# Performance work log

Hardware: AMD Instinct MI355X
Metric: run time of the kernel (lower is better)

Reference implementation:

```python
import jax, jax.numpy as jnp
import numpy as np

D_MODEL = 1024
N_HEADS = 16
D_HEAD = D_MODEL // N_HEADS


def setup_inputs() -> dict:
    key = jax.random.key(0)
    ks = jax.random.split(key, 9)
    s = 1.0 / np.sqrt(D_MODEL)
    def lin(kw, kb):
        W = jax.random.uniform(kw, (D_MODEL, D_MODEL), jnp.float32, -s, s)
        b = jax.random.uniform(kb, (D_MODEL,), jnp.float32, -s, s)
        return W, b
    Wq, bq = lin(ks[0], ks[1])
    Wk, bk = lin(ks[2], ks[3])
    Wv, bv = lin(ks[4], ks[5])
    Wo, bo = lin(ks[6], ks[7])
    x = jax.random.normal(ks[8], (4, 2048, D_MODEL), jnp.float32)
    return {"x": x, "Wq": Wq, "bq": bq, "Wk": Wk, "bk": bk,
            "Wv": Wv, "bv": bv, "Wo": Wo, "bo": bo}


def reference(x, Wq, bq, Wk, bk, Wv, bv, Wo, bo):
    B, T, C = x.shape
    # torch Linear: y = x @ W.T + b
    Q = x @ Wq.T + bq
    K = x @ Wk.T + bk
    V = x @ Wv.T + bv
    # [B, H, T, Dh]
    Q = Q.reshape(B, T, N_HEADS, D_HEAD).transpose(0, 2, 1, 3)
    K = K.reshape(B, T, N_HEADS, D_HEAD).transpose(0, 2, 1, 3)
    V = V.reshape(B, T, N_HEADS, D_HEAD).transpose(0, 2, 1, 3)
    scale = jnp.float32(np.sqrt(D_HEAD))
    scores = jnp.einsum('bhqd,bhkd->bhqk', Q, K) / scale
    causal = jnp.tril(jnp.ones((T, T), dtype=bool))  # True where allowed
    scores = jnp.where(causal, scores, jnp.float32(-jnp.inf))
    attn = jax.nn.softmax(scores, axis=-1)
    out = jnp.einsum('bhqk,bhkd->bhqd', attn, V)
    out = out.transpose(0, 2, 1, 3).reshape(B, T, C)
    return out @ Wo.T + bo
```

## Files before the change

kernel.cpp:

```cpp
#include <hip/hip_runtime.h>
#include <hip/hip_bf16.h>


typedef float f32x4 __attribute__((ext_vector_type(4)));
typedef __bf16 bf16x8 __attribute__((ext_vector_type(8)));

#define DEVI __device__ __forceinline__

#define QSCALE 0.1803368801111204f

DEVI ushort f2b(float x) {
  __hip_bfloat16 h = __float2bfloat16(x);
  return __builtin_bit_cast(ushort, h);
}

DEVI bf16x8 ldsFrag(const ushort* p) {
  return __builtin_bit_cast(bf16x8, *(const uint4*)p);
}

DEVI f32x4 mfma16(bf16x8 a, bf16x8 b, f32x4 c) {
  return __builtin_amdgcn_mfma_f32_16x16x32_bf16(a, b, c, 0, 0, 0);
}

DEVI void gload_lds16(const ushort* g, ushort* l) {
  __builtin_amdgcn_global_load_lds(
      (const __attribute__((address_space(1))) unsigned int*)g,
      (__attribute__((address_space(3))) unsigned int*)l, 16, 0, 0);
}

__global__ void k_cvt(const float4* __restrict__ in, ushort4* __restrict__ out, int n4) {
  int i = blockIdx.x * 256 + threadIdx.x;
  if (i >= n4) return;
  float4 f = in[i];
  ushort4 o;
  o.x = f2b(f.x); o.y = f2b(f.y); o.z = f2b(f.z); o.w = f2b(f.w);
  out[i] = o;
}

__global__ void k_cvtW(const float4* __restrict__ w0, const float4* __restrict__ w1,
                       const float4* __restrict__ w2, const float4* __restrict__ w3,
                       ushort4* __restrict__ out) {
  const int y = blockIdx.y;
  const float4* src = (y == 0) ? w0 : (y == 1) ? w1 : (y == 2) ? w2 : w3;
  const int i = blockIdx.x * 256 + threadIdx.x;
  float4 f = src[i];
  ushort4 o;
  o.x = f2b(f.x); o.y = f2b(f.y); o.z = f2b(f.z); o.w = f2b(f.w);
  out[y * 262144 + i] = o;
}

template<int MODE>
__global__ __launch_bounds__(256)
void k_gemm(const ushort* __restrict__ A, const ushort* __restrict__ W,
            const float* __restrict__ b0, const float* __restrict__ b1,
            const float* __restrict__ b2, float* __restrict__ outF,
            ushort* __restrict__ oQ, ushort* __restrict__ oK, ushort* __restrict__ oV) {
  __shared__ ushort As[128 * 32];
  __shared__ ushort Bs[128 * 32];
  const int tid = threadIdx.x;
  const int wave = tid >> 6, lane = tid & 63;
  const int col = lane & 15, quad = lane >> 4;
  const int m0 = blockIdx.y * 128, n0 = blockIdx.x * 128;
  const int wm = (wave >> 1) * 64, wn = (wave & 1) * 64;
  f32x4 acc[4][4] = {};

  const int srow = wave * 16 + (lane >> 2);
  const int scol = (lane & 3) * 8;
  const ushort* Ag = A + (m0 + srow) * 1024 + scol;
  const ushort* Wg = W + (n0 + srow) * 1024 + scol;
  ushort* AsBase0 = &As[(wave * 16) * 32];
  ushort* AsBase1 = &As[(64 + wave * 16) * 32];
  ushort* BsBase0 = &Bs[(wave * 16) * 32];
  ushort* BsBase1 = &Bs[(64 + wave * 16) * 32];

  for (int k0 = 0; k0 < 1024; k0 += 32) {
    __syncthreads();
    gload_lds16(Ag + k0,             AsBase0);
    gload_lds16(Ag + 64 * 1024 + k0, AsBase1);
    gload_lds16(Wg + k0,             BsBase0);
    gload_lds16(Wg + 64 * 1024 + k0, BsBase1);
    __syncthreads();

    bf16x8 af[4], bfr[4];
#pragma unroll
    for (int i = 0; i < 4; ++i)
      af[i] = ldsFrag(&As[(wm + i * 16 + col) * 32 + quad * 8]);
#pragma unroll
    for (int j = 0; j < 4; ++j)
      bfr[j] = ldsFrag(&Bs[(wn + j * 16 + col) * 32 + quad * 8]);
#pragma unroll
    for (int i = 0; i < 4; ++i)
#pragma unroll
      for (int j = 0; j < 4; ++j)
        acc[i][j] = mfma16(af[i], bfr[j], acc[i][j]);
  }

  const int matId = (MODE == 0) ? (n0 >> 10) : 0;
  const float* bias = (MODE == 1) ? b0 : (matId == 0 ? b0 : (matId == 1 ? b1 : b2));
  const float sc = (MODE == 0 && matId == 0) ? QSCALE : 1.0f;
  ushort* outB = (MODE == 0) ? (matId == 0 ? oQ : (matId == 1 ? oK : oV)) : nullptr;

#pragma unroll
  for (int j = 0; j < 4; ++j) {
    const int n = n0 + wn + j * 16 + col;
    const int nl = n & 1023;
    const float bn = bias[nl];
#pragma unroll
    for (int i = 0; i < 4; ++i) {
      const int mBase = m0 + wm + i * 16 + quad * 4;
      if (MODE == 1) {
#pragma unroll
        for (int r = 0; r < 4; ++r)
          outF[(mBase + r) * 1024 + n] = acc[i][j][r] + bn;
      } else if (matId < 2) {
        const int h = nl >> 6, dh = nl & 63;
#pragma unroll
        for (int r = 0; r < 4; ++r) {
          const int m = mBase + r;
          const int b = m >> 11, t = m & 2047;
          outB[(((b * 16 + h) * 2048) + t) * 64 + dh] = f2b((acc[i][j][r] + bn) * sc);
        }
      } else {
        const int b = mBase >> 11, t = mBase & 2047;
        const int h = nl >> 6, dh = nl & 63;
        ushort4 pk;
        pk.x = f2b(acc[i][j][0] + bn);
        pk.y = f2b(acc[i][j][1] + bn);
        pk.z = f2b(acc[i][j][2] + bn);
        pk.w = f2b(acc[i][j][3] + bn);
        *(ushort4*)&outB[(((b * 16 + h) * 64) + dh) * 2048 + t] = pk;
      }
    }
  }
}

__global__ __launch_bounds__(256)
void k_attn(const ushort* __restrict__ Q, const ushort* __restrict__ K,
            const ushort* __restrict__ Vt, ushort* __restrict__ AO) {
  __shared__ ushort Ks[2 * 64 * 32];
  __shared__ ushort Vs[2 * 64 * 32];
  __shared__ ushort Ps[4 * 16 * 72];
  const int tid = threadIdx.x;
  const int wave = tid >> 6, lane = tid & 63;
  const int col = lane & 15, quad = lane >> 4;
  const int bh = blockIdx.y;
  const int px = blockIdx.x;
  const ushort* Qg = Q + (size_t)bh * 2048 * 64;
  const ushort* Kg = K + (size_t)bh * 2048 * 64;
  const ushort* Vg = Vt + (size_t)bh * 64 * 2048;

  const int srow = wave * 16 + (lane >> 2);
  const int scol = (lane & 3) * 8;
  ushort* Ks0 = &Ks[(wave * 16) * 32];
  ushort* Ks1 = &Ks[(64 + wave * 16) * 32];
  ushort* Vs0 = &Vs[(wave * 16) * 32];
  ushort* Vs1 = &Vs[(64 + wave * 16) * 32];
  ushort* Pw = &Ps[wave * 16 * 72 + col * 72];

  for (int pp = 0; pp < 2; ++pp) {
    const int t = pp ? (31 - px) : px;
    const int q0 = t * 64;
    const int qw = q0 + wave * 16;

    bf16x8 qf0, qf1;
    {
      const ushort* p = Qg + (qw + col) * 64 + quad * 8;
      qf0 = __builtin_bit_cast(bf16x8, *(const uint4*)p);
      qf1 = __builtin_bit_cast(bf16x8, *(const uint4*)(p + 32));
    }

    float mrow = -1e30f, lsum = 0.0f;
    f32x4 o[4] = {};

    const ushort* kPtr = Kg + srow * 64 + scol;
    const ushort* vPtr = Vg + srow * 2048 + scol;

    for (int it = 0; it <= t; ++it) {
      __syncthreads();
      gload_lds16(kPtr,      Ks0);
      gload_lds16(kPtr + 32, Ks1);
      gload_lds16(vPtr,      Vs0);
      gload_lds16(vPtr + 32, Vs1);
      kPtr += 64 * 64;
      vPtr += 64;
      __syncthreads();

      const bool diag = (it == t);
      const int imax = diag ? wave : 3;

      f32x4 p[4];
      float tmax = -1e30f;
#pragma unroll
      for (int i = 0; i < 4; ++i) {
        if (i > imax) { p[i] = f32x4{0.f, 0.f, 0.f, 0.f}; continue; }
        bf16x8 kf0 = ldsFrag(&Ks[(i * 16 + col) * 32 + quad * 8]);
        bf16x8 kf1 = ldsFrag(&Ks[(64 + i * 16 + col) * 32 + quad * 8]);
        f32x4 z = {0.f, 0.f, 0.f, 0.f};
        f32x4 s = mfma16(kf0, qf0, z);
        s = mfma16(kf1, qf1, s);
        if (diag && i == wave) {
#pragma unroll
          for (int r = 0; r < 4; ++r)
            if (quad * 4 + r > col) s[r] = -1e30f;
        }
#pragma unroll
        for (int r = 0; r < 4; ++r) tmax = fmaxf(tmax, s[r]);
        p[i] = s;
      }
      tmax = fmaxf(tmax, __shfl_xor(tmax, 16));
      tmax = fmaxf(tmax, __shfl_xor(tmax, 32));
      const float mnew = fmaxf(mrow, tmax);
      const float alpha = __builtin_amdgcn_exp2f(mrow - mnew);
      float psum = 0.0f;
#pragma unroll
      for (int i = 0; i < 4; ++i) {
        if (i > imax) continue;
#pragma unroll
        for (int r = 0; r < 4; ++r) {
          const float e = __builtin_amdgcn_exp2f(p[i][r] - mnew);
          p[i][r] = e;
          psum += e;
        }
      }
      psum += __shfl_xor(psum, 16);
      psum += __shfl_xor(psum, 32);
      lsum = alpha * lsum + psum;
      mrow = mnew;
#pragma unroll
      for (int i = 0; i < 4; ++i) o[i] *= alpha;

#pragma unroll
      for (int i = 0; i < 4; ++i) {
        ushort4 pk;
        pk.x = f2b(p[i][0]); pk.y = f2b(p[i][1]);
        pk.z = f2b(p[i][2]); pk.w = f2b(p[i][3]);
        *(ushort4*)&Pw[i * 16 + quad * 4] = pk;
      }

#pragma unroll
      for (int c = 0; c < 2; ++c) {
        bf16x8 pb = ldsFrag(&Pw[c * 32 + quad * 8]);
#pragma unroll
        for (int i = 0; i < 4; ++i) {
          bf16x8 vf = ldsFrag(&Vs[(c * 64 + i * 16 + col) * 32 + quad * 8]);
          o[i] = mfma16(vf, pb, o[i]);
        }
      }
    }

    const float inv = 1.0f / lsum;
    const int b = bh >> 4, h = bh & 15;
    const int tq = q0 + wave * 16 + col;
    ushort* dst = AO + ((size_t)(b * 2048 + tq)) * 1024 + h * 64;
#pragma unroll
    for (int i = 0; i < 4; ++i) {
      ushort4 pk;
      pk.x = f2b(o[i][0] * inv);
      pk.y = f2b(o[i][1] * inv);
      pk.z = f2b(o[i][2] * inv);
      pk.w = f2b(o[i][3] * inv);
      *(ushort4*)&dst[i * 16 + quad * 4] = pk;
    }
  }
}

extern "C" void kernel_launch(void* const* d_in, const int* in_sizes, int n_in,
                              void* d_out, int out_size, void* d_ws, size_t ws_size,
                              hipStream_t stream) {
  const float* x  = (const float*)d_in[0];
  const float* Wq = (const float*)d_in[1];
  const float* bq = (const float*)d_in[2];
  const float* Wk = (const float*)d_in[3];
  const float* bk = (const float*)d_in[4];
  const float* Wv = (const float*)d_in[5];
  const float* bv = (const float*)d_in[6];
  const float* Wo = (const float*)d_in[7];
  const float* bo = (const float*)d_in[8];
  float* out = (float*)d_out;

  char* ws = (char*)d_ws;
  ushort* xb    = (ushort*)ws;
  ushort* Wcat  = (ushort*)(ws + (size_t)16 * 1024 * 1024);
  ushort* Wob   = Wcat + (size_t)3 * 1024 * 1024;
  ushort* Qh    = (ushort*)(ws + (size_t)24 * 1024 * 1024);
  ushort* Kh    = Qh + (size_t)8192 * 1024;
  ushort* Vt    = Kh + (size_t)8192 * 1024;
  ushort* AO    = Vt + (size_t)8192 * 1024;

  k_cvt<<<8192, 256, 0, stream>>>((const float4*)x, (ushort4*)xb, 8192 * 1024 / 4);
  k_cvtW<<<dim3(1024, 4), 256, 0, stream>>>((const float4*)Wq, (const float4*)Wk,
                                            (const float4*)Wv, (const float4*)Wo,
                                            (ushort4*)Wcat);

  k_gemm<0><<<dim3(24, 64), 256, 0, stream>>>(xb, Wcat, bq, bk, bv, nullptr, Qh, Kh, Vt);

  k_attn<<<dim3(16, 64), 256, 0, stream>>>(Qh, Kh, Vt, AO);

  k_gemm<1><<<dim3(8, 64), 256, 0, stream>>>(AO, Wob, bo, nullptr, nullptr, out,
                                             nullptr, nullptr, nullptr);
}
```

Before: 285.5 us.

## Restructure attention to 128-query tiles, MFMA row sums, and swizzled block mapping

Each attention block now handles 128 queries, with two 16-row query sub-tiles per wave, so every staged K/V tile is reused across twice as many queries. Row sums are computed by an MFMA against a ones block appended to the V tile instead of shuffle reductions. Blocks are remapped with a 1D swizzle across XCDs for both GEMMs and attention, and attention gets a launch_bounds occupancy hint. The cost is more registers and LDS per block and lost load balance, since the old pairing of short and long causal tiles is dropped.

```diff
diff --git a/kernel.cpp b/kernel.cpp
--- a/kernel.cpp
+++ b/kernel.cpp
@@ -12,6 +12,12 @@
 DEVI ushort f2b(float x) {
   __hip_bfloat16 h = __float2bfloat16(x);
   return __builtin_bit_cast(ushort, h);
+}
+
+DEVI ushort4 pack4(f32x4 v) {
+  ushort4 o;
+  o.x = f2b(v[0]); o.y = f2b(v[1]); o.z = f2b(v[2]); o.w = f2b(v[3]);
+  return o;
 }
 
 DEVI bf16x8 ldsFrag(const ushort* p) {
@@ -60,7 +66,10 @@
   const int tid = threadIdx.x;
   const int wave = tid >> 6, lane = tid & 63;
   const int col = lane & 15, quad = lane >> 4;
-  const int m0 = blockIdx.y * 128, n0 = blockIdx.x * 128;
+  const int id = blockIdx.x;
+  const int s_ = id >> 3;
+  const int m0 = ((id & 7) * 8 + (s_ & 7)) * 128;
+  const int n0 = (s_ >> 3) * 128;
   const int wm = (wave >> 1) * 64, wn = (wave & 1) * 64;
   f32x4 acc[4][4] = {};
 
@@ -134,132 +143,160 @@
   }
 }
 
-__global__ __launch_bounds__(256)
+__global__ __launch_bounds__(256, 3)
 void k_attn(const ushort* __restrict__ Q, const ushort* __restrict__ K,
             const ushort* __restrict__ Vt, ushort* __restrict__ AO) {
   __shared__ ushort Ks[2 * 64 * 32];
-  __shared__ ushort Vs[2 * 64 * 32];
-  __shared__ ushort Ps[4 * 16 * 72];
+  __shared__ ushort Vs[2 * 80 * 32];
+  __shared__ ushort Ps[4 * 2 * 16 * 72];
   const int tid = threadIdx.x;
   const int wave = tid >> 6, lane = tid & 63;
   const int col = lane & 15, quad = lane >> 4;
-  const int bh = blockIdx.y;
-  const int px = blockIdx.x;
+  const int id = blockIdx.x;
+  const int sl = id >> 3;
+  const int bh = (id & 7) * 8 + (sl & 7);
+  const int t = sl >> 3;
+  const int q0 = t * 128;
   const ushort* Qg = Q + (size_t)bh * 2048 * 64;
   const ushort* Kg = K + (size_t)bh * 2048 * 64;
   const ushort* Vg = Vt + (size_t)bh * 64 * 2048;
 
+  {
+    const int c = tid >> 7, w = tid & 127;
+    const ushort one = 0x3F80;
+    ushort4 zv;
+    if (w < 8) { zv.x = one; zv.y = one; zv.z = one; zv.w = one; }
+    else       { zv.x = 0;   zv.y = 0;   zv.z = 0;   zv.w = 0;   }
+    *(ushort4*)&Vs[c * 2560 + 2048 + w * 4] = zv;
+  }
+
+  bf16x8 qf[2][2];
+#pragma unroll
+  for (int s = 0; s < 2; ++s) {
+    const ushort* p = Qg + (q0 + wave * 32 + s * 16 + col) * 64 + quad * 8;
+    qf[s][0] = __builtin_bit_cast(bf16x8, *(const uint4*)p);
+    qf[s][1] = __builtin_bit_cast(bf16x8, *(const uint4*)(p + 32));
+  }
+
+  float mrow[2] = {-1e30f, -1e30f};
+  f32x4 o[2][4] = {};
+  f32x4 la[2] = {};
+
   const int srow = wave * 16 + (lane >> 2);
   const int scol = (lane & 3) * 8;
+  const ushort* kPtr = Kg + srow * 64 + scol;
+  const ushort* vPtr = Vg + srow * 2048 + scol;
   ushort* Ks0 = &Ks[(wave * 16) * 32];
   ushort* Ks1 = &Ks[(64 + wave * 16) * 32];
   ushort* Vs0 = &Vs[(wave * 16) * 32];
-  ushort* Vs1 = &Vs[(64 + wave * 16) * 32];
-  ushort* Pw = &Ps[wave * 16 * 72 + col * 72];
-
-  for (int pp = 0; pp < 2; ++pp) {
-    const int t = pp ? (31 - px) : px;
-    const int q0 = t * 64;
-    const int qw = q0 + wave * 16;
-
-    bf16x8 qf0, qf1;
-    {
-      const ushort* p = Qg + (qw + col) * 64 + quad * 8;
-      qf0 = __builtin_bit_cast(bf16x8, *(const uint4*)p);
-      qf1 = __builtin_bit_cast(bf16x8, *(const uint4*)(p + 32));
-    }
-
-    float mrow = -1e30f, lsum = 0.0f;
-    f32x4 o[4] = {};
-
-    const ushort* kPtr = Kg + srow * 64 + scol;
-    const ushort* vPtr = Vg + srow * 2048 + scol;
-
-    for (int it = 0; it <= t; ++it) {
-      __syncthreads();
-      gload_lds16(kPtr,      Ks0);
-      gload_lds16(kPtr + 32, Ks1);
-      gload_lds16(vPtr,      Vs0);
-      gload_lds16(vPtr + 32, Vs1);
-      kPtr += 64 * 64;
-      vPtr += 64;
-      __syncthreads();
-
-      const bool diag = (it == t);
-      const int imax = diag ? wave : 3;
-
+  ushort* Vs1 = &Vs[2560 + (wave * 16) * 32];
+  ushort* Pw0 = &Ps[((wave * 2 + 0) * 16 + col) * 72];
+  ushort* Pw1 = &Ps[((wave * 2 + 1) * 16 + col) * 72];
+
+  auto stage = [&]() {
+    gload_lds16(kPtr,      Ks0);
+    gload_lds16(kPtr + 32, Ks1);
+    gload_lds16(vPtr,      Vs0);
+    gload_lds16(vPtr + 32, Vs1);
+    kPtr += 64 * 64;
+    vPtr += 64;
+  };
+
+  auto step = [&](bool masked, int d) {
+    bf16x8 kf[4][2];
+#pragma unroll
+    for (int i = 0; i < 4; ++i) {
+      kf[i][0] = ldsFrag(&Ks[(i * 16 + col) * 32 + quad * 8]);
+      kf[i][1] = ldsFrag(&Ks[(64 + i * 16 + col) * 32 + quad * 8]);
+    }
+#pragma unroll
+    for (int s = 0; s < 2; ++s) {
+      const int exact = masked ? (2 * wave + s - 4 * d) : 99;
       f32x4 p[4];
       float tmax = -1e30f;
 #pragma unroll
       for (int i = 0; i < 4; ++i) {
-        if (i > imax) { p[i] = f32x4{0.f, 0.f, 0.f, 0.f}; continue; }
-        bf16x8 kf0 = ldsFrag(&Ks[(i * 16 + col) * 32 + quad * 8]);
-        bf16x8 kf1 = ldsFrag(&Ks[(64 + i * 16 + col) * 32 + quad * 8]);
-        f32x4 z = {0.f, 0.f, 0.f, 0.f};
-        f32x4 s = mfma16(kf0, qf0, z);
-        s = mfma16(kf1, qf1, s);
-        if (diag && i == wave) {
-#pragma unroll
-          for (int r = 0; r < 4; ++r)
-            if (quad * 4 + r > col) s[r] = -1e30f;
+        if (i <= exact) {
+          f32x4 z = {0.f, 0.f, 0.f, 0.f};
+          f32x4 sv = mfma16(kf[i][0], qf[s][0], z);
+          sv = mfma16(kf[i][1], qf[s][1], sv);
+          if (masked && i == exact) {
+#pragma unroll
+            for (int r = 0; r < 4; ++r)
+              if (quad * 4 + r > col) sv[r] = -1e30f;
+          }
+#pragma unroll
+          for (int r = 0; r < 4; ++r) tmax = fmaxf(tmax, sv[r]);
+          p[i] = sv;
+        } else {
+          p[i] = f32x4{0.f, 0.f, 0.f, 0.f};
         }
-#pragma unroll
-        for (int r = 0; r < 4; ++r) tmax = fmaxf(tmax, s[r]);
-        p[i] = s;
       }
       tmax = fmaxf(tmax, __shfl_xor(tmax, 16));
       tmax = fmaxf(tmax, __shfl_xor(tmax, 32));
-      const float mnew = fmaxf(mrow, tmax);
-      const float alpha = __builtin_amdgcn_exp2f(mrow - mnew);
-      float psum = 0.0f;
+      const float mnew = fmaxf(mrow[s], tmax);
+      const float alpha = __builtin_amdgcn_exp2f(mrow[s] - mnew);
+      mrow[s] = mnew;
 #pragma unroll
       for (int i = 0; i < 4; ++i) {
-        if (i > imax) continue;
-#pragma unroll
-        for (int r = 0; r < 4; ++r) {
-          const float e = __builtin_amdgcn_exp2f(p[i][r] - mnew);
-          p[i][r] = e;
-          psum += e;
+        if (i <= exact) {
+#pragma unroll
+          for (int r = 0; r < 4; ++r)
+            p[i][r] = __builtin_amdgcn_exp2f(p[i][r] - mnew);
         }
       }
-      psum += __shfl_xor(psum, 16);
-      psum += __shfl_xor(psum, 32);
-      lsum = alpha * lsum + psum;
-      mrow = mnew;
-#pragma unroll
-      for (int i = 0; i < 4; ++i) o[i] *= alpha;
-
+      la[s] *= alpha;
+#pragma unroll
+      for (int i = 0; i < 4; ++i) o[s][i] *= alpha;
+      ushort* Pw = s ? Pw1 : Pw0;
+#pragma unroll
+      for (int i = 0; i < 4; ++i)
+        *(ushort4*)&Pw[i * 16 + quad * 4] = pack4(p[i]);
+    }
+#pragma unroll
+    for (int c = 0; c < 2; ++c) {
+      bf16x8 pb0 = ldsFrag(&Pw0[c * 32 + quad * 8]);
+      bf16x8 pb1 = ldsFrag(&Pw1[c * 32 + quad * 8]);
+      bf16x8 vone = ldsFrag(&Vs[(c * 80 + 64 + col) * 32 + quad * 8]);
+      la[0] = mfma16(vone, pb0, la[0]);
+      la[1] = mfma16(vone, pb1, la[1]);
 #pragma unroll
       for (int i = 0; i < 4; ++i) {
-        ushort4 pk;
-        pk.x = f2b(p[i][0]); pk.y = f2b(p[i][1]);
-        pk.z = f2b(p[i][2]); pk.w = f2b(p[i][3]);
-        *(ushort4*)&Pw[i * 16 + quad * 4] = pk;
+        bf16x8 vf = ldsFrag(&Vs[(c * 80 + i * 16 + col) * 32 + quad * 8]);
+        o[0][i] = mfma16(vf, pb0, o[0][i]);
+        o[1][i] = mfma16(vf, pb1, o[1][i]);
       }
-
-#pragma unroll
-      for (int c = 0; c < 2; ++c) {
-        bf16x8 pb = ldsFrag(&Pw[c * 32 + quad * 8]);
-#pragma unroll
-        for (int i = 0; i < 4; ++i) {
-          bf16x8 vf = ldsFrag(&Vs[(c * 64 + i * 16 + col) * 32 + quad * 8]);
-          o[i] = mfma16(vf, pb, o[i]);
-        }
-      }
-    }
-
-    const float inv = 1.0f / lsum;
-    const int b = bh >> 4, h = bh & 15;
-    const int tq = q0 + wave * 16 + col;
-    ushort* dst = AO + ((size_t)(b * 2048 + tq)) * 1024 + h * 64;
+    }
+  };
+
+  const int nfull = 2 * t;
+  for (int it = 0; it < nfull; ++it) {
+    __syncthreads();
+    stage();
+    __syncthreads();
+    step(false, 0);
+  }
+  __syncthreads();
+  stage();
+  __syncthreads();
+  step(true, 0);
+  __syncthreads();
+  stage();
+  __syncthreads();
+  if (wave >= 2) step(true, 1);
+
+  const int b = bh >> 4, h = bh & 15;
+#pragma unroll
+  for (int s = 0; s < 2; ++s) {
+    const float l = __shfl(la[s][0], col);
+    const float inv = 1.0f / l;
+    const int tq = q0 + wave * 32 + s * 16 + col;
+    ushort* dst = AO + (size_t)(b * 2048 + tq) * 1024 + h * 64;
 #pragma unroll
     for (int i = 0; i < 4; ++i) {
-      ushort4 pk;
-      pk.x = f2b(o[i][0] * inv);
-      pk.y = f2b(o[i][1] * inv);
-      pk.z = f2b(o[i][2] * inv);
-      pk.w = f2b(o[i][3] * inv);
-      *(ushort4*)&dst[i * 16 + quad * 4] = pk;
+      f32x4 v = o[s][i];
+      v[0] *= inv; v[1] *= inv; v[2] *= inv; v[3] *= inv;
+      *(ushort4*)&dst[i * 16 + quad * 4] = pack4(v);
     }
   }
 }
@@ -292,10 +329,10 @@
                                             (const float4*)Wv, (const float4*)Wo,
                                             (ushort4*)Wcat);
 
-  k_gemm<0><<<dim3(24, 64), 256, 0, stream>>>(xb, Wcat, bq, bk, bv, nullptr, Qh, Kh, Vt);
-
-  k_attn<<<dim3(16, 64), 256, 0, stream>>>(Qh, Kh, Vt, AO);
-
-  k_gemm<1><<<dim3(8, 64), 256, 0, stream>>>(AO, Wob, bo, nullptr, nullptr, out,
-                                             nullptr, nullptr, nullptr);
-}
+  k_gemm<0><<<1536, 256, 0, stream>>>(xb, Wcat, bq, bk, bv, nullptr, Qh, Kh, Vt);
+
+  k_attn<<<1024, 256, 0, stream>>>(Qh, Kh, Vt, AO);
+
+  k_gemm<1><<<512, 256, 0, stream>>>(AO, Wob, bo, nullptr, nullptr, out,
+                                     nullptr, nullptr, nullptr);
+}
```

After: 268.3 us. -6.0%, faster.
